# Performance work log

Hardware: AMD Instinct MI355X
Metric: run time of the kernel (lower is better)

The kernel has to match this reference:

```python
import jax, jax.numpy as jnp
import numpy as np

N = 50000   # nodes
E = 800000  # edges
D = 128     # embed_dim
H = 8       # num_heads
DK = D // H # d_k = 16


def _xavier(k, shape):
    lim = np.sqrt(6.0 / (shape[0] + shape[1])).astype(np.float32)
    return jax.random.uniform(k, shape, jnp.float32, -lim, lim)


def setup_inputs() -> dict:
    key = jax.random.key(0)
    ks = jax.random.split(key, 8)
    x = jax.random.normal(ks[0], (N, D), jnp.float32)
    edge_index = jax.random.randint(ks[1], (2, E), 0, N, jnp.int64)
    att_bias = jax.random.normal(ks[2], (E, H), jnp.float32)
    # Linear weights stored as [in, out] (torch stores [out, in]; math identical)
    Wq = _xavier(ks[3], (D, D)); bq = jnp.zeros((D,), jnp.float32)
    Wk = _xavier(ks[4], (D, D)); bk = jnp.zeros((D,), jnp.float32)
    Wv = _xavier(ks[5], (D, D)); bv = jnp.zeros((D,), jnp.float32)
    Wo = _xavier(ks[6], (D, D)); bo = jnp.zeros((D,), jnp.float32)
    return {"x": x, "edge_index": edge_index, "att_bias": att_bias,
            "Wq": Wq, "bq": bq, "Wk": Wk, "bk": bk,
            "Wv": Wv, "bv": bv, "Wo": Wo, "bo": bo}


def reference(x, edge_index, att_bias, Wq, bq, Wk, bk, Wv, bv, Wo, bo):
    n = x.shape[0]
    e = edge_index.shape[1]
    h = att_bias.shape[1]
    dk = Wq.shape[1] // h
    dst = edge_index[0]  # query-side node per edge (segment ids)
    src = edge_index[1]  # key/value-side node per edge

    # project on nodes (N x D GEMMs), then gather per edge -> [E, H, DK]
    q = (x @ Wq + bq)[dst].reshape(e, h, dk)
    k = (x @ Wk + bk)[src].reshape(e, h, dk)
    v = (x @ Wv + bv)[src].reshape(e, h, dk)

    scale = 1.0 / np.sqrt(dk).astype(np.float32)
    logits = scale * jnp.sum(q * k, axis=2, keepdims=True)  # [E, H, 1]
    logits = logits + att_bias[..., None]

    # segmented (scatter) softmax over edges grouped by dst node
    seg_max = jax.ops.segment_max(logits, dst, num_segments=n)   # [N, H, 1]
    ex = jnp.exp(logits - seg_max[dst])
    seg_sum = jax.ops.segment_sum(ex, dst, num_segments=n)        # [N, H, 1]
    scores = ex / seg_sum[dst]                                    # [E, H, 1]

    # weighted scatter-sum aggregation -> [N, H, DK]
    agg = jax.ops.segment_sum(scores * v, dst, num_segments=n)
    out = agg.reshape(n, h * dk) @ Wo + bo                        # [N, D]
    return out, logits
```

## Files before the change

kernel.cpp:

```cpp
#include <hip/hip_runtime.h>
#include <hip/hip_bf16.h>
#include <math.h>


typedef __bf16 bf16x8 __attribute__((ext_vector_type(8)));
typedef float  f32x4  __attribute__((ext_vector_type(4)));

__device__ __forceinline__ ushort f32_to_bf16(float f) {
    uint u = __float_as_uint(f);
    u += 0x7FFF + ((u >> 16) & 1);
    return (ushort)(u >> 16);
}
__device__ __forceinline__ uint pack_bf16x2(float a, float b) {
    return (uint)f32_to_bf16(a) | ((uint)f32_to_bf16(b) << 16);
}
__device__ __forceinline__ float bf_lo(uint w) { return __uint_as_float(w << 16); }
__device__ __forceinline__ float bf_hi(uint w) { return __uint_as_float(w & 0xFFFF0000u); }

template<int LDC, bool OUT_BF16>
__global__ __launch_bounds__(256) void gemm_mfma(
    const ushort* __restrict__ A, const ushort* __restrict__ Bt,
    const float* __restrict__ bias, void* __restrict__ Cv, int M)
{
    __shared__ uint4 As4[2048];
    __shared__ uint4 Bs4[2048];
    const int tid  = threadIdx.x;
    const int wave = tid >> 6;
    const int lane = tid & 63;
    const int qd   = lane >> 4;
    const int ln   = lane & 15;
    const int rowBase = blockIdx.x * 128;
    const int colBase = blockIdx.y * 128;

    const uint4* gA = (const uint4*)(A + (size_t)rowBase * 128);
    #pragma unroll
    for (int i = 0; i < 8; ++i) {
        int c  = tid + i * 256;
        int lc = (c & ~15) | ((c ^ (c >> 4)) & 15);
        As4[lc] = gA[c];
    }
    const uint4* gB = (const uint4*)(Bt + (size_t)colBase * 128);
    #pragma unroll
    for (int i = 0; i < 8; ++i) {
        int c  = tid + i * 256;
        int lc = (c & ~15) | ((c ^ (c >> 4)) & 15);
        Bs4[lc] = gB[c];
    }
    __syncthreads();

    f32x4 acc[2][8];
    #pragma unroll
    for (int i = 0; i < 2; ++i)
        #pragma unroll
        for (int j = 0; j < 8; ++j)
            acc[i][j] = (f32x4){0.f, 0.f, 0.f, 0.f};

    const int m0 = wave * 32;
    #pragma unroll
    for (int ks = 0; ks < 4; ++ks) {
        const int kc = ks * 4 + qd;
        bf16x8 a0 = *((const bf16x8*)&As4[(m0 +      ln) * 16 + (kc ^ ln)]);
        bf16x8 a1 = *((const bf16x8*)&As4[(m0 + 16 + ln) * 16 + (kc ^ ln)]);
        #pragma unroll
        for (int j = 0; j < 8; ++j) {
            bf16x8 b = *((const bf16x8*)&Bs4[(j * 16 + ln) * 16 + (kc ^ ln)]);
            acc[0][j] = __builtin_amdgcn_mfma_f32_16x16x32_bf16(b, a0, acc[0][j], 0, 0, 0);
            acc[1][j] = __builtin_amdgcn_mfma_f32_16x16x32_bf16(b, a1, acc[1][j], 0, 0, 0);
        }
    }

    #pragma unroll
    for (int i = 0; i < 2; ++i) {
        int gr = rowBase + m0 + i * 16 + ln;
        if (gr < M) {
            #pragma unroll
            for (int j = 0; j < 8; ++j) {
                int coln = colBase + j * 16 + qd * 4;
                float4 b4 = *((const float4*)(bias + coln));
                float v0 = acc[i][j][0] + b4.x;
                float v1 = acc[i][j][1] + b4.y;
                float v2 = acc[i][j][2] + b4.z;
                float v3 = acc[i][j][3] + b4.w;
                if (OUT_BF16) {
                    uint2 o;
                    o.x = pack_bf16x2(v0, v1);
                    o.y = pack_bf16x2(v2, v3);
                    *((uint2*)((ushort*)Cv + (size_t)gr * LDC + coln)) = o;
                } else {
                    float4 o = make_float4(v0, v1, v2, v3);
                    *((float4*)((float*)Cv + (size_t)gr * LDC + coln)) = o;
                }
            }
        }
    }
}

__global__ __launch_bounds__(256) void prep_kernel(
    const float* __restrict__ x,
    const float* __restrict__ Wq, const float* __restrict__ Wk,
    const float* __restrict__ Wv, const float* __restrict__ bq,
    const float* __restrict__ bk, const float* __restrict__ bv,
    const float* __restrict__ Wo,
    ushort* __restrict__ WcatT, float* __restrict__ bcatI, ushort* __restrict__ WoT,
    ushort* __restrict__ xb, int* __restrict__ cnt, int N, int Mpad, int GSZ)
{
    const int gid = blockIdx.x * 256 + threadIdx.x;

    for (int i = gid; i < N; i += GSZ) cnt[i] = 0;

    const int WTOT = 384 * 128 + 384 + 128 * 128;
    for (int idx = gid; idx < WTOT; idx += GSZ) {
        if (idx < 384 * 128) {
            int jj = idx >> 7, k = idx & 127;
            const float* W; int c;
            if (jj < 128) { W = Wq; c = jj; }
            else {
                int t = jj - 128;
                int chunk = t >> 3, pos = t & 7;
                int h = chunk >> 2, g = chunk & 3;
                c = h * 16 + g * 4 + (pos & 3);
                W = (pos < 4) ? Wk : Wv;
            }
            WcatT[idx] = f32_to_bf16(W[k * 128 + c]);
        } else if (idx < 384 * 128 + 384) {
            int jj = idx - 384 * 128;
            float b;
            if (jj < 128) b = bq[jj];
            else {
                int t = jj - 128;
                int chunk = t >> 3, pos = t & 7;
                int h = chunk >> 2, g = chunk & 3;
                int c = h * 16 + g * 4 + (pos & 3);
                b = (pos < 4) ? bk[c] : bv[c];
            }
            bcatI[jj] = b;
        } else {
            int t = idx - (384 * 128 + 384);
            int n = t >> 7, k = t & 127;
            WoT[t] = f32_to_bf16(Wo[k * 128 + n]);
        }
    }

    for (int i = gid; i < Mpad * 32; i += GSZ) {
        int r = i >> 5;
        ushort4 o;
        if (r < N) {
            float4 v = ((const float4*)x)[i];
            o.x = f32_to_bf16(v.x); o.y = f32_to_bf16(v.y);
            o.z = f32_to_bf16(v.z); o.w = f32_to_bf16(v.w);
        } else {
            o.x = o.y = o.z = o.w = 0;
        }
        ((ushort4*)xb)[i] = o;
    }
}

__global__ void hist_kernel(const int* __restrict__ dst, int* __restrict__ cnt,
                            int* __restrict__ rank, int E)
{
    int e = blockIdx.x * 256 + threadIdx.x;
    if (e < E) rank[e] = atomicAdd(&cnt[dst[e]], 1);
}

__global__ __launch_bounds__(256) void scan_block(const int* __restrict__ cnt,
                                                  int* __restrict__ incl,
                                                  int* __restrict__ bsum, int N)
{
    __shared__ int sd[256];
    int tid = threadIdx.x;
    int i = blockIdx.x * 256 + tid;
    int v = (i < N) ? cnt[i] : 0;
    sd[tid] = v;
    __syncthreads();
    #pragma unroll
    for (int o = 1; o < 256; o <<= 1) {
        int t = (tid >= o) ? sd[tid - o] : 0;
        __syncthreads();
        sd[tid] += t;
        __syncthreads();
    }
    if (i < N) incl[i] = sd[tid];
    if (tid == 255) bsum[blockIdx.x] = sd[255];
}

__global__ __launch_bounds__(256) void scan_finish(
    const int* __restrict__ cnt, const int* __restrict__ incl,
    const int* __restrict__ bsum, int* __restrict__ offp,
    int N, int E, int nblk)
{
    __shared__ int sd[256];
    __shared__ int pfx;
    int tid = threadIdx.x;
    int v = (tid < nblk) ? bsum[tid] : 0;
    sd[tid] = v;
    __syncthreads();
    #pragma unroll
    for (int o = 1; o < 256; o <<= 1) {
        int t = (tid >= o) ? sd[tid - o] : 0;
        __syncthreads();
        sd[tid] += t;
        __syncthreads();
    }
    if (tid == blockIdx.x) pfx = sd[tid] - v;
    __syncthreads();
    int i = blockIdx.x * 256 + tid;
    if (i < N) offp[i] = incl[i] - cnt[i] + pfx;
    if (i == 0) offp[N] = E;
}

__global__ void scatter_kernel(const int* __restrict__ dst, const int* __restrict__ srcs,
                               const int* __restrict__ rank, const int* __restrict__ offp,
                               int2* __restrict__ pairs, const float* __restrict__ att_bias,
                               float* __restrict__ biasS, int E, int useS)
{
    int e = blockIdx.x * 256 + threadIdx.x;
    if (e < E) {
        int slot = offp[dst[e]] + rank[e];
        pairs[slot] = make_int2(srcs[e], e);
        if (useS) {
            float4 b0 = ((const float4*)att_bias)[e * 2];
            float4 b1 = ((const float4*)att_bias)[e * 2 + 1];
            ((float4*)biasS)[(size_t)slot * 2]     = b0;
            ((float4*)biasS)[(size_t)slot * 2 + 1] = b1;
        }
    }
}

__global__ __launch_bounds__(256) void attn_kernel(
    const ushort* __restrict__ Cb, const int* __restrict__ off,
    const int2* __restrict__ pairs, const float* __restrict__ att_bias,
    const float* __restrict__ biasS, int useS,
    float* __restrict__ logits_out, ushort* __restrict__ aggb, int N)
{
    const int wv   = threadIdx.x >> 6;
    const int lane = threadIdx.x & 63;
    const int node = blockIdx.x * 4 + wv;
    if (node >= N) return;
    const int e2 = lane >> 5;
    const int c  = lane & 31;
    const int h  = c >> 2;

    uint2 qw = ((const uint2*)(Cb + (size_t)node * 384))[c];
    const float q0 = bf_lo(qw.x), q1 = bf_hi(qw.x);
    const float q2 = bf_lo(qw.y), q3 = bf_hi(qw.y);

    const int s = off[node];
    const int e = off[node + 1];
    const char* cb = (const char*)Cb;

    float l = 0.f, a0 = 0.f, a1 = 0.f, a2 = 0.f, a3 = 0.f;

    for (int b0 = s; b0 < e; b0 += 64) {
        const int cnt = min(64, e - b0);
        int gidx = b0 + ((lane < cnt) ? lane : (cnt - 1));
        int2 se = pairs[gidx];
        int  regEid = se.y;
        uint regOff = (uint)se.x * 768u + 256u;

        const int npairs = cnt >> 1;
        int t = 0;
        for (; t + 4 <= npairs; t += 4) {
            int  e4[4]; uint o4[4];
            uint4 w4[4]; float b4[4];
            #pragma unroll
            for (int j = 0; j < 4; ++j) {
                int idx = 2 * (t + j) + e2;
                e4[j] = __shfl(regEid, idx);
                o4[j] = __shfl(regOff, idx);
            }
            #pragma unroll
            for (int j = 0; j < 4; ++j) {
                w4[j] = *((const uint4*)(cb + o4[j]) + c);
                b4[j] = useS ? biasS[(uint)(b0 + 2 * (t + j) + e2) * 8u + h]
                             : att_bias[e4[j] * 8 + h];
            }
            #pragma unroll
            for (int j = 0; j < 4; ++j) {
                uint4 w = w4[j];
                float p = q0 * bf_lo(w.x) + q1 * bf_hi(w.x)
                        + q2 * bf_lo(w.y) + q3 * bf_hi(w.y);
                p += __shfl_xor(p, 1);
                p += __shfl_xor(p, 2);
                float logit = p * 0.25f + b4[j];
                if ((c & 3) == 0) logits_out[e4[j] * 8 + h] = logit;
                float pe = __expf(logit);
                l += pe;
                a0 = fmaf(pe, bf_lo(w.z), a0); a1 = fmaf(pe, bf_hi(w.z), a1);
                a2 = fmaf(pe, bf_lo(w.w), a2); a3 = fmaf(pe, bf_hi(w.w), a3);
            }
        }
        for (; t < npairs; ++t) {
            int idx = 2 * t + e2;
            int  ei = __shfl(regEid, idx);
            uint of = __shfl(regOff, idx);
            uint4 w = *((const uint4*)(cb + of) + c);
            float bb = useS ? biasS[(uint)(b0 + idx) * 8u + h]
                            : att_bias[ei * 8 + h];
            float p = q0 * bf_lo(w.x) + q1 * bf_hi(w.x)
                    + q2 * bf_lo(w.y) + q3 * bf_hi(w.y);
            p += __shfl_xor(p, 1);
            p += __shfl_xor(p, 2);
            float logit = p * 0.25f + bb;
            if ((c & 3) == 0) logits_out[ei * 8 + h] = logit;
            float pe = __expf(logit);
            l += pe;
            a0 = fmaf(pe, bf_lo(w.z), a0); a1 = fmaf(pe, bf_hi(w.z), a1);
            a2 = fmaf(pe, bf_lo(w.w), a2); a3 = fmaf(pe, bf_hi(w.w), a3);
        }
        if (cnt & 1) {
            int idx = cnt - 1;
            int  ei = __shfl(regEid, idx);
            uint of = __shfl(regOff, idx);
            uint4 w = *((const uint4*)(cb + of) + c);
            float bb = useS ? biasS[(uint)(b0 + idx) * 8u + h]
                            : att_bias[ei * 8 + h];
            float p = q0 * bf_lo(w.x) + q1 * bf_hi(w.x)
                    + q2 * bf_lo(w.y) + q3 * bf_hi(w.y);
            p += __shfl_xor(p, 1);
            p += __shfl_xor(p, 2);
            float logit = p * 0.25f + bb;
            if ((c & 3) == 0 && e2 == 0) logits_out[ei * 8 + h] = logit;
            float pe = (e2 == 0) ? __expf(logit) : 0.f;
            l += pe;
            a0 = fmaf(pe, bf_lo(w.z), a0); a1 = fmaf(pe, bf_hi(w.z), a1);
            a2 = fmaf(pe, bf_lo(w.w), a2); a3 = fmaf(pe, bf_hi(w.w), a3);
        }
    }

    l  += __shfl_xor(l, 32);
    a0 += __shfl_xor(a0, 32);
    a1 += __shfl_xor(a1, 32);
    a2 += __shfl_xor(a2, 32);
    a3 += __shfl_xor(a3, 32);
    float inv = (l > 0.f) ? (1.f / l) : 0.f;
    if (e2 == 0) {
        uint2 o;
        o.x = pack_bf16x2(a0 * inv, a1 * inv);
        o.y = pack_bf16x2(a2 * inv, a3 * inv);
        ((uint2*)(aggb + (size_t)node * 128))[c] = o;
    }
}

extern "C" void kernel_launch(void* const* d_in, const int* in_sizes, int n_in,
                              void* d_out, int out_size, void* d_ws, size_t ws_size,
                              hipStream_t stream)
{
    const float* x        = (const float*)d_in[0];
    const int*   ei       = (const int*)d_in[1];
    const float* att_bias = (const float*)d_in[2];
    const float* Wq = (const float*)d_in[3];  const float* bq = (const float*)d_in[4];
    const float* Wk = (const float*)d_in[5];  const float* bk = (const float*)d_in[6];
    const float* Wv = (const float*)d_in[7];  const float* bv = (const float*)d_in[8];
    const float* Wo = (const float*)d_in[9];  const float* bo = (const float*)d_in[10];

    const int N = in_sizes[0] / 128;
    const int E = in_sizes[1] / 2;

    float* out    = (float*)d_out;
    float* logits = out + (size_t)N * 128;

    char* ws = (char*)d_ws;
    size_t o = 0;
    auto alloc = [&](size_t bytes) -> char* {
        char* p = ws + o;
        o = (o + bytes + 255) & ~(size_t)255;
        return p;
    };
    const int Mpad = ((N + 127) / 128) * 128;
    ushort* Cb    = (ushort*)alloc((size_t)N * 384 * 2);
    ushort* aggb  = (ushort*)alloc((size_t)Mpad * 128 * 2);
    ushort* xb    = (ushort*)alloc((size_t)Mpad * 128 * 2);
    ushort* WcatT = (ushort*)alloc((size_t)384 * 128 * 2);
    float*  bcatI = (float*)alloc(384 * 4);
    ushort* WoT   = (ushort*)alloc((size_t)128 * 128 * 2);
    int*    cnt   = (int*)alloc((size_t)N * 4);
    int*    incl  = (int*)alloc((size_t)N * 4);
    int*    rank  = (int*)alloc((size_t)E * 4);
    const int NBLK = (N + 255) / 256;
    int*    bsum  = (int*)alloc((size_t)NBLK * 4);
    int*    offp  = (int*)alloc((size_t)(N + 1) * 4);
    int2*   pairs = (int2*)alloc((size_t)E * 8);
    float*  biasS = (float*)alloc((size_t)E * 8 * 4);
    const int useS = (o <= ws_size) ? 1 : 0;
    if (!useS) biasS = nullptr;

    const int MB  = (N + 127) / 128;
    const int nbE = (E + 255) / 256;

    const int PREP_BLOCKS = 1024;
    prep_kernel<<<PREP_BLOCKS, 256, 0, stream>>>(
        x, Wq, Wk, Wv, bq, bk, bv, Wo, WcatT, bcatI, WoT, xb, cnt,
        N, Mpad, PREP_BLOCKS * 256);

    dim3 g1(MB, 3);
    gemm_mfma<384, true><<<g1, 256, 0, stream>>>(xb, WcatT, bcatI, Cb, N);

    hist_kernel<<<nbE, 256, 0, stream>>>(ei, cnt, rank, E);
    scan_block<<<NBLK, 256, 0, stream>>>(cnt, incl, bsum, N);
    scan_finish<<<NBLK, 256, 0, stream>>>(cnt, incl, bsum, offp, N, E, NBLK);
    scatter_kernel<<<nbE, 256, 0, stream>>>(ei, ei + E, rank, offp, pairs,
                                            att_bias, biasS, E, useS);

    attn_kernel<<<(N + 3) / 4, 256, 0, stream>>>(Cb, offp, pairs, att_bias,
                                                 biasS, useS, logits, aggb, N);

    dim3 g2(MB, 1);
    gemm_mfma<128, false><<<g2, 256, 0, stream>>>(aggb, WoT, bo, out, N);
}
```

Baseline: 298.3 us.

## Use plain K/V layout and process four edges per wavefront with 8-wide lanes

Drops the interleaved K/V column permutation in the projected weight layout, so K and V sit in separate contiguous 256-byte blocks per node. The attention kernel now handles four edges per iteration with 16 lanes per edge, each lane covering 8 elements, where before it handled two edges with 32 lanes of 4 elements. This halves the shuffle reduction depth and removes the unrolled pair loop and its tail cases. In exchange, each edge costs two 16-byte gathers instead of one, there is no 4-deep unroll to hide load latency, and lanes past the edge count do wasted work in partial groups.

```diff
diff --git a/kernel.cpp b/kernel.cpp
--- a/kernel.cpp
+++ b/kernel.cpp
@@ -113,26 +113,16 @@
         if (idx < 384 * 128) {
             int jj = idx >> 7, k = idx & 127;
             const float* W; int c;
-            if (jj < 128) { W = Wq; c = jj; }
-            else {
-                int t = jj - 128;
-                int chunk = t >> 3, pos = t & 7;
-                int h = chunk >> 2, g = chunk & 3;
-                c = h * 16 + g * 4 + (pos & 3);
-                W = (pos < 4) ? Wk : Wv;
-            }
+            if (jj < 128)      { W = Wq; c = jj; }
+            else if (jj < 256) { W = Wk; c = jj - 128; }
+            else               { W = Wv; c = jj - 256; }
             WcatT[idx] = f32_to_bf16(W[k * 128 + c]);
         } else if (idx < 384 * 128 + 384) {
             int jj = idx - 384 * 128;
             float b;
-            if (jj < 128) b = bq[jj];
-            else {
-                int t = jj - 128;
-                int chunk = t >> 3, pos = t & 7;
-                int h = chunk >> 2, g = chunk & 3;
-                int c = h * 16 + g * 4 + (pos & 3);
-                b = (pos < 4) ? bk[c] : bv[c];
-            }
+            if (jj < 128)      b = bq[jj];
+            else if (jj < 256) b = bk[jj - 128];
+            else               b = bv[jj - 256];
             bcatI[jj] = b;
         } else {
             int t = idx - (384 * 128 + 384);
@@ -236,108 +226,77 @@
     const int lane = threadIdx.x & 63;
     const int node = blockIdx.x * 4 + wv;
     if (node >= N) return;
-    const int e2 = lane >> 5;
-    const int c  = lane & 31;
-    const int h  = c >> 2;
-
-    uint2 qw = ((const uint2*)(Cb + (size_t)node * 384))[c];
+    const int eg   = lane >> 4;
+    const int r    = lane & 15;
+    const int h    = r >> 1;
+    const int half = lane & 1;
+
+    const char* cb = (const char*)Cb;
+
+    uint4 qw = *((const uint4*)(cb + (size_t)node * 768) + r);
     const float q0 = bf_lo(qw.x), q1 = bf_hi(qw.x);
     const float q2 = bf_lo(qw.y), q3 = bf_hi(qw.y);
+    const float q4 = bf_lo(qw.z), q5 = bf_hi(qw.z);
+    const float q6 = bf_lo(qw.w), q7 = bf_hi(qw.w);
 
     const int s = off[node];
     const int e = off[node + 1];
-    const char* cb = (const char*)Cb;
-
-    float l = 0.f, a0 = 0.f, a1 = 0.f, a2 = 0.f, a3 = 0.f;
+
+    float l = 0.f;
+    float a0 = 0.f, a1 = 0.f, a2 = 0.f, a3 = 0.f;
+    float a4 = 0.f, a5 = 0.f, a6 = 0.f, a7 = 0.f;
 
     for (int b0 = s; b0 < e; b0 += 64) {
         const int cnt = min(64, e - b0);
         int gidx = b0 + ((lane < cnt) ? lane : (cnt - 1));
         int2 se = pairs[gidx];
-        int  regEid = se.y;
-        uint regOff = (uint)se.x * 768u + 256u;
-
-        const int npairs = cnt >> 1;
-        int t = 0;
-        for (; t + 4 <= npairs; t += 4) {
-            int  e4[4]; uint o4[4];
-            uint4 w4[4]; float b4[4];
-            #pragma unroll
-            for (int j = 0; j < 4; ++j) {
-                int idx = 2 * (t + j) + e2;
-                e4[j] = __shfl(regEid, idx);
-                o4[j] = __shfl(regOff, idx);
-            }
-            #pragma unroll
-            for (int j = 0; j < 4; ++j) {
-                w4[j] = *((const uint4*)(cb + o4[j]) + c);
-                b4[j] = useS ? biasS[(uint)(b0 + 2 * (t + j) + e2) * 8u + h]
-                             : att_bias[e4[j] * 8 + h];
-            }
-            #pragma unroll
-            for (int j = 0; j < 4; ++j) {
-                uint4 w = w4[j];
-                float p = q0 * bf_lo(w.x) + q1 * bf_hi(w.x)
-                        + q2 * bf_lo(w.y) + q3 * bf_hi(w.y);
-                p += __shfl_xor(p, 1);
-                p += __shfl_xor(p, 2);
-                float logit = p * 0.25f + b4[j];
-                if ((c & 3) == 0) logits_out[e4[j] * 8 + h] = logit;
-                float pe = __expf(logit);
-                l += pe;
-                a0 = fmaf(pe, bf_lo(w.z), a0); a1 = fmaf(pe, bf_hi(w.z), a1);
-                a2 = fmaf(pe, bf_lo(w.w), a2); a3 = fmaf(pe, bf_hi(w.w), a3);
-            }
-        }
-        for (; t < npairs; ++t) {
-            int idx = 2 * t + e2;
-            int  ei = __shfl(regEid, idx);
-            uint of = __shfl(regOff, idx);
-            uint4 w = *((const uint4*)(cb + of) + c);
-            float bb = useS ? biasS[(uint)(b0 + idx) * 8u + h]
-                            : att_bias[ei * 8 + h];
-            float p = q0 * bf_lo(w.x) + q1 * bf_hi(w.x)
-                    + q2 * bf_lo(w.y) + q3 * bf_hi(w.y);
+        int regSrc = se.x;
+        int regEid = se.y;
+
+        for (int g = 0; g < cnt; g += 4) {
+            int  idxr  = g + eg;
+            bool valid = idxr < cnt;
+            int  idxc  = valid ? idxr : (cnt - 1);
+            int  srcn  = __shfl(regSrc, idxc);
+            int  eid   = __shfl(regEid, idxc);
+            const char* kv = cb + (size_t)((uint)srcn * 768u);
+            uint4 kw = *((const uint4*)(kv + 256) + r);
+            uint4 vw = *((const uint4*)(kv + 512) + r);
+            float bb = useS ? biasS[(uint)(b0 + idxc) * 8u + h]
+                            : att_bias[eid * 8 + h];
+
+            float p = q0 * bf_lo(kw.x) + q1 * bf_hi(kw.x)
+                    + q2 * bf_lo(kw.y) + q3 * bf_hi(kw.y)
+                    + q4 * bf_lo(kw.z) + q5 * bf_hi(kw.z)
+                    + q6 * bf_lo(kw.w) + q7 * bf_hi(kw.w);
             p += __shfl_xor(p, 1);
-            p += __shfl_xor(p, 2);
             float logit = p * 0.25f + bb;
-            if ((c & 3) == 0) logits_out[ei * 8 + h] = logit;
-            float pe = __expf(logit);
+            if (valid && half == 0) logits_out[eid * 8 + h] = logit;
+            float pe = valid ? __expf(logit) : 0.f;
             l += pe;
-            a0 = fmaf(pe, bf_lo(w.z), a0); a1 = fmaf(pe, bf_hi(w.z), a1);
-            a2 = fmaf(pe, bf_lo(w.w), a2); a3 = fmaf(pe, bf_hi(w.w), a3);
-        }
-        if (cnt & 1) {
-            int idx = cnt - 1;
-            int  ei = __shfl(regEid, idx);
-            uint of = __shfl(regOff, idx);
-            uint4 w = *((const uint4*)(cb + of) + c);
-            float bb = useS ? biasS[(uint)(b0 + idx) * 8u + h]
-                            : att_bias[ei * 8 + h];
-            float p = q0 * bf_lo(w.x) + q1 * bf_hi(w.x)
-                    + q2 * bf_lo(w.y) + q3 * bf_hi(w.y);
-            p += __shfl_xor(p, 1);
-            p += __shfl_xor(p, 2);
-            float logit = p * 0.25f + bb;
-            if ((c & 3) == 0 && e2 == 0) logits_out[ei * 8 + h] = logit;
-            float pe = (e2 == 0) ? __expf(logit) : 0.f;
-            l += pe;
-            a0 = fmaf(pe, bf_lo(w.z), a0); a1 = fmaf(pe, bf_hi(w.z), a1);
-            a2 = fmaf(pe, bf_lo(w.w), a2); a3 = fmaf(pe, bf_hi(w.w), a3);
-        }
-    }
-
-    l  += __shfl_xor(l, 32);
-    a0 += __shfl_xor(a0, 32);
-    a1 += __shfl_xor(a1, 32);
-    a2 += __shfl_xor(a2, 32);
-    a3 += __shfl_xor(a3, 32);
+            a0 = fmaf(pe, bf_lo(vw.x), a0); a1 = fmaf(pe, bf_hi(vw.x), a1);
+            a2 = fmaf(pe, bf_lo(vw.y), a2); a3 = fmaf(pe, bf_hi(vw.y), a3);
+            a4 = fmaf(pe, bf_lo(vw.z), a4); a5 = fmaf(pe, bf_hi(vw.z), a5);
+            a6 = fmaf(pe, bf_lo(vw.w), a6); a7 = fmaf(pe, bf_hi(vw.w), a7);
+        }
+    }
+
+    #pragma unroll
+    for (int m = 16; m <= 32; m <<= 1) {
+        l  += __shfl_xor(l, m);
+        a0 += __shfl_xor(a0, m); a1 += __shfl_xor(a1, m);
+        a2 += __shfl_xor(a2, m); a3 += __shfl_xor(a3, m);
+        a4 += __shfl_xor(a4, m); a5 += __shfl_xor(a5, m);
+        a6 += __shfl_xor(a6, m); a7 += __shfl_xor(a7, m);
+    }
     float inv = (l > 0.f) ? (1.f / l) : 0.f;
-    if (e2 == 0) {
-        uint2 o;
+    if (eg == 0) {
+        uint4 o;
         o.x = pack_bf16x2(a0 * inv, a1 * inv);
         o.y = pack_bf16x2(a2 * inv, a3 * inv);
-        ((uint2*)(aggb + (size_t)node * 128))[c] = o;
+        o.z = pack_bf16x2(a4 * inv, a5 * inv);
+        o.w = pack_bf16x2(a6 * inv, a7 * inv);
+        ((uint4*)(aggb + (size_t)node * 128))[r] = o;
     }
 }
 
```

After: 296.3 us. About the same (-0.7%).
